# Performance work log

Measured on AMD Instinct MI355X. Metric: run time of the kernel, lower is better.

The kernel has to match this reference:

```python
import jax, jax.numpy as jnp
import numpy as np


def setup_inputs() -> dict:
    key = jax.random.key(0)
    B = 64          # number of utterances (segments)
    N = 16384       # total frames = sum(segment_num)
    D = 1024        # embedding_size
    A = 2048        # attention_dim
    H = 8           # attention_head_num
    k1, k2, k3, k4 = jax.random.split(key, 4)
    # ragged segment lengths, all >= 1, summing exactly to N
    rng = np.random.default_rng(0)
    lens = rng.integers(64, 512, size=B).astype(np.float64)
    lens = np.maximum(1, (lens * N / lens.sum()).astype(np.int64))
    lens[-1] += N - lens.sum()
    assert lens.sum() == N and (lens > 0).all()
    segment_num = jnp.asarray(lens, dtype=jnp.int32)
    x = jax.random.normal(k1, (N, D), jnp.float32)
    # torch Linear weights, stored pre-transposed as [in, out]
    w1 = jax.random.normal(k2, (D, A), jnp.float32) / np.sqrt(D)
    w2 = jax.random.normal(k3, (A, H), jnp.float32) / np.sqrt(A)
    # post_fc: Linear(D*H -> D, bias=False), stored as [D*H, D]
    w_post = jax.random.normal(k4, (D * H, D), jnp.float32) / np.sqrt(D * H)
    return {"x": x, "segment_num": segment_num, "w1": w1, "w2": w2, "w_post": w_post}


def reference(x, segment_num, w1, w2, w_post):
    N, D = x.shape
    B = segment_num.shape[0]
    H = w2.shape[1]
    # segment id for every frame (ragged -> flat segment ids)
    seg_ids = jnp.repeat(jnp.arange(B), segment_num, total_repeat_length=N)  # [N]

    # MultiAtt.w1: Linear -> ReLU -> Linear, per frame
    h = jnp.maximum(x @ w1, 0.0) @ w2  # [N, H]

    # per-segment softmax over the time axis (dim 0 within each segment)
    m = jax.ops.segment_max(h, seg_ids, num_segments=B)          # [B, H]
    p = jnp.exp(h - m[seg_ids])                                  # [N, H]
    s = jax.ops.segment_sum(p, seg_ids, num_segments=B)          # [B, H]
    attn = p / s[seg_ids]                                        # [N, H]

    # per-segment x^T @ attn -> [B, D, H] (matches torch.mm(x.T, attn))
    out_bdh = jax.ops.segment_sum(x[:, :, None] * attn[:, None, :], seg_ids, num_segments=B)
    # flatten row-major over (D, H) like out.view(-1), then post_fc (no bias)
    out = out_bdh.reshape(B, D * H) @ w_post                     # [B, D]

    # attn_i = attn^T @ attn per segment -> [B, H, H]
    attn_gram = jax.ops.segment_sum(attn[:, :, None] * attn[:, None, :], seg_ids, num_segments=B)

    # segment_type == 'average': per-segment mean of frames -> [B, D]
    out_segment = jax.ops.segment_sum(x, seg_ids, num_segments=B) / segment_num[:, None].astype(x.dtype)

    return out, out_segment, attn_gram
```

## Files before the change

kernel.cpp:

```cpp
#include <hip/hip_runtime.h>
#include <hip/hip_bf16.h>

#define NB 64
#define NN 16384
#define ND 1024
#define NA 2048
#define NH 8
#define NSLOT 16
#define KSPL 64
#define NPL 16

typedef __attribute__((ext_vector_type(4))) float f32x4;
typedef __attribute__((ext_vector_type(8))) short short8;
typedef __attribute__((ext_vector_type(8))) unsigned short ushort8;

__device__ __forceinline__ unsigned short f2bf(float f) {
    unsigned int u = __float_as_uint(f);
    u = (u + 0x7fff + ((u >> 16) & 1)) >> 16;
    return (unsigned short)u;
}

__device__ __forceinline__ float bf2f(unsigned short s) {
    return __uint_as_float((unsigned int)s << 16);
}

__device__ __forceinline__ void load_lds16(const void* g, void* l) {
    __builtin_amdgcn_global_load_lds((const __attribute__((address_space(1))) void*)g,
                                     (__attribute__((address_space(3))) void*)l, 16, 0, 0);
}

__global__ __launch_bounds__(256) void k_pre(const float* __restrict__ x,
                                             const float* __restrict__ w1,
                                             const int* __restrict__ segnum,
                                             unsigned short* __restrict__ xb,
                                             unsigned short* __restrict__ w1t,
                                             int* __restrict__ segoff) {
    __shared__ unsigned short t[32][33];
    const int bx = blockIdx.x;
    if (bx < 8192) {
        size_t i = ((size_t)bx * 256 + threadIdx.x) * 8;
        float4 a = *(const float4*)(x + i);
        float4 b = *(const float4*)(x + i + 4);
        ushort8 o;
        o[0] = f2bf(a.x); o[1] = f2bf(a.y); o[2] = f2bf(a.z); o[3] = f2bf(a.w);
        o[4] = f2bf(b.x); o[5] = f2bf(b.y); o[6] = f2bf(b.z); o[7] = f2bf(b.w);
        *(ushort8*)(xb + i) = o;
    } else if (bx < 10240) {
        const int idx = bx - 8192;
        const int a0 = (idx & 63) * 32, d0 = (idx >> 6) * 32;
        const int tx = threadIdx.x & 31, ty4 = (threadIdx.x >> 5) * 4;
#pragma unroll
        for (int i = 0; i < 4; i++)
            t[tx][ty4 + i] = f2bf(w1[(size_t)(d0 + ty4 + i) * NA + a0 + tx]);
        __syncthreads();
#pragma unroll
        for (int i = 0; i < 4; i++)
            w1t[(size_t)(a0 + ty4 + i) * ND + d0 + tx] = t[ty4 + i][tx];
    } else {
        if (threadIdx.x == 0) {
            int a = 0;
            segoff[0] = 0;
            for (int b = 0; b < NB; b++) { a += segnum[b]; segoff[b + 1] = a; }
        }
    }
}

__global__ __launch_bounds__(256) void k_c1h(const unsigned short* __restrict__ xb,
                                             const unsigned short* __restrict__ w1t,
                                             const float* __restrict__ w2,
                                             float* __restrict__ h_part) {
    __shared__ unsigned short SM[21760];
    unsigned short* As  = SM;
    unsigned short* Bs  = SM + 8192;
    unsigned short* c1s = SM;
    unsigned short* w2hi = SM + 17408;
    unsigned short* w2lo = SM + 19584;

    const int tid = threadIdx.x;
    const int wave = tid >> 6, lane = tid & 63;
    const int wm = wave & 1, wn = wave >> 1;
    const int m0 = blockIdx.x * 128, n0 = blockIdx.y * 128;
    const int quad = lane >> 4, lc = lane & 15;

    for (int i = tid; i < 2176; i += 256) { w2hi[i] = 0; w2lo[i] = 0; }
    for (int i = tid; i < 1024; i += 256) {
        int k = i >> 3, q = i & 7;
        float w = w2[(size_t)(n0 + k) * NH + q];
        unsigned short hi = f2bf(w);
        w2hi[q * 136 + k] = hi;
        w2lo[q * 136 + k] = f2bf(w - bf2f(hi));
    }

    f32x4 acc[4][4];
#pragma unroll
    for (int i = 0; i < 4; i++)
#pragma unroll
        for (int j = 0; j < 4; j++) acc[i][j] = (f32x4){0.f, 0.f, 0.f, 0.f};

    const int srow = lane >> 3;
    const int sg = lane & 7;

    for (int k0 = 0; k0 < ND; k0 += 64) {
        __syncthreads();
#pragma unroll
        for (int i = 0; i < 4; i++) {
            int r = wave * 32 + i * 8 + srow;
            int gc = (sg ^ (r & 7)) * 8;
            load_lds16(xb + (size_t)(m0 + r) * ND + k0 + gc, As + r * 64 + sg * 8);
            load_lds16(w1t + (size_t)(n0 + r) * ND + k0 + gc, Bs + r * 64 + sg * 8);
        }
        __syncthreads();
#pragma unroll
        for (int ksub = 0; ksub < 2; ksub++) {
            short8 af[4], bf[4];
            const int lg = ksub * 4 + quad;
#pragma unroll
            for (int t = 0; t < 4; t++) {
                int m = wm * 64 + t * 16 + lc;
                af[t] = *(const short8*)&As[m * 64 + (lg ^ (m & 7)) * 8];
                int n = wn * 64 + t * 16 + lc;
                bf[t] = *(const short8*)&Bs[n * 64 + (lg ^ (n & 7)) * 8];
            }
#pragma unroll
            for (int mi = 0; mi < 4; mi++)
#pragma unroll
                for (int ni = 0; ni < 4; ni++)
                    acc[mi][ni] = __builtin_amdgcn_mfma_f32_16x16x32_bf16(
                        af[mi], bf[ni], acc[mi][ni], 0, 0, 0);
        }
    }

    __syncthreads();
#pragma unroll
    for (int mi = 0; mi < 4; mi++)
#pragma unroll
        for (int ni = 0; ni < 4; ni++) {
            const int col = wn * 64 + ni * 16 + lc;
#pragma unroll
            for (int r = 0; r < 4; r++) {
                const int row = wm * 64 + mi * 16 + quad * 4 + r;
                c1s[row * 136 + col] = f2bf(fmaxf(acc[mi][ni][r], 0.f));
            }
        }
    __syncthreads();

    f32x4 hacc[2];
    hacc[0] = (f32x4){0.f, 0.f, 0.f, 0.f};
    hacc[1] = (f32x4){0.f, 0.f, 0.f, 0.f};
#pragma unroll
    for (int ks = 0; ks < 4; ks++) {
        short8 bh = *(const short8*)&w2hi[lc * 136 + ks * 32 + quad * 8];
        short8 bl = *(const short8*)&w2lo[lc * 136 + ks * 32 + quad * 8];
#pragma unroll
        for (int mt = 0; mt < 2; mt++) {
            short8 af = *(const short8*)&c1s[(wave * 32 + mt * 16 + lc) * 136 + ks * 32 + quad * 8];
            hacc[mt] = __builtin_amdgcn_mfma_f32_16x16x32_bf16(af, bh, hacc[mt], 0, 0, 0);
            hacc[mt] = __builtin_amdgcn_mfma_f32_16x16x32_bf16(af, bl, hacc[mt], 0, 0, 0);
        }
    }

    if (lc < NH) {
        float* hp = h_part + (size_t)blockIdx.y * (NN * NH);
#pragma unroll
        for (int mt = 0; mt < 2; mt++)
#pragma unroll
            for (int r = 0; r < 4; r++)
                hp[(size_t)(m0 + wave * 32 + mt * 16 + quad * 4 + r) * NH + lc] = hacc[mt][r];
    }
}

__global__ __launch_bounds__(256) void k_attn(const float* __restrict__ h_part,
                                              float* __restrict__ attn,
                                              const int* __restrict__ segoff,
                                              float* __restrict__ gram) {
    const int b = blockIdx.x;
    const int s0 = segoff[b], s1 = segoff[b + 1];
    const int len = s1 - s0;
    const int tid = threadIdx.x;
    const int wv = tid >> 6;
    __shared__ float hl[1024 * NH];
    __shared__ float red[4][NH];
    __shared__ float mb[NH];
    __shared__ float sinv[NH];
    __shared__ float gred[4][64];

    float mx[NH];
#pragma unroll
    for (int q = 0; q < NH; q++) mx[q] = -1e30f;

    const bool cached = (len <= 1024);

    for (int n = s0 + tid; n < s1; n += 256) {
        float v[NH];
#pragma unroll
        for (int q = 0; q < NH; q++) v[q] = 0.f;
#pragma unroll
        for (int p = 0; p < NPL; p++) {
            const float4* hp = (const float4*)(h_part + (size_t)p * (NN * NH) + (size_t)n * NH);
            float4 u0 = hp[0], u1 = hp[1];
            v[0] += u0.x; v[1] += u0.y; v[2] += u0.z; v[3] += u0.w;
            v[4] += u1.x; v[5] += u1.y; v[6] += u1.z; v[7] += u1.w;
        }
        if (cached) {
#pragma unroll
            for (int q = 0; q < NH; q++) hl[(n - s0) * NH + q] = v[q];
        }
#pragma unroll
        for (int q = 0; q < NH; q++) mx[q] = fmaxf(mx[q], v[q]);
    }
#pragma unroll
    for (int q = 0; q < NH; q++)
        for (int o = 1; o < 64; o <<= 1) mx[q] = fmaxf(mx[q], __shfl_xor(mx[q], o));
    if ((tid & 63) == 0)
        for (int q = 0; q < NH; q++) red[wv][q] = mx[q];
    __syncthreads();
    if (tid < NH)
        mb[tid] = fmaxf(fmaxf(red[0][tid], red[1][tid]), fmaxf(red[2][tid], red[3][tid]));
    __syncthreads();

    float sm[NH];
#pragma unroll
    for (int q = 0; q < NH; q++) sm[q] = 0.f;
    for (int n = s0 + tid; n < s1; n += 256) {
        float v[NH];
        if (cached) {
#pragma unroll
            for (int q = 0; q < NH; q++) v[q] = hl[(n - s0) * NH + q];
        } else {
#pragma unroll
            for (int q = 0; q < NH; q++) v[q] = 0.f;
#pragma unroll
            for (int p = 0; p < NPL; p++) {
                const float4* hp = (const float4*)(h_part + (size_t)p * (NN * NH) + (size_t)n * NH);
                float4 u0 = hp[0], u1 = hp[1];
                v[0] += u0.x; v[1] += u0.y; v[2] += u0.z; v[3] += u0.w;
                v[4] += u1.x; v[5] += u1.y; v[6] += u1.z; v[7] += u1.w;
            }
        }
#pragma unroll
        for (int q = 0; q < NH; q++) sm[q] += expf(v[q] - mb[q]);
    }
#pragma unroll
    for (int q = 0; q < NH; q++)
        for (int o = 1; o < 64; o <<= 1) sm[q] += __shfl_xor(sm[q], o);
    if ((tid & 63) == 0)
        for (int q = 0; q < NH; q++) red[wv][q] = sm[q];
    __syncthreads();
    if (tid < NH)
        sinv[tid] = 1.0f / (red[0][tid] + red[1][tid] + red[2][tid] + red[3][tid]);
    __syncthreads();

    float g[NH][NH];
#pragma unroll
    for (int i = 0; i < NH; i++)
#pragma unroll
        for (int j = 0; j < NH; j++) g[i][j] = 0.f;

    for (int n = s0 + tid; n < s1; n += 256) {
        float v[NH];
        if (cached) {
#pragma unroll
            for (int q = 0; q < NH; q++) v[q] = hl[(n - s0) * NH + q];
        } else {
#pragma unroll
            for (int q = 0; q < NH; q++) v[q] = 0.f;
#pragma unroll
            for (int p = 0; p < NPL; p++) {
                const float4* hp = (const float4*)(h_part + (size_t)p * (NN * NH) + (size_t)n * NH);
                float4 u0 = hp[0], u1 = hp[1];
                v[0] += u0.x; v[1] += u0.y; v[2] += u0.z; v[3] += u0.w;
                v[4] += u1.x; v[5] += u1.y; v[6] += u1.z; v[7] += u1.w;
            }
        }
        float a[NH];
        float* ar = &attn[(size_t)n * NH];
#pragma unroll
        for (int q = 0; q < NH; q++) { a[q] = expf(v[q] - mb[q]) * sinv[q]; ar[q] = a[q]; }
#pragma unroll
        for (int i = 0; i < NH; i++)
#pragma unroll
            for (int j = 0; j < NH; j++) g[i][j] += a[i] * a[j];
    }
#pragma unroll
    for (int i = 0; i < NH; i++)
#pragma unroll
        for (int j = 0; j < NH; j++)
            for (int o = 1; o < 64; o <<= 1) g[i][j] += __shfl_xor(g[i][j], o);

    if ((tid & 63) == 0) {
#pragma unroll
        for (int i = 0; i < NH; i++)
#pragma unroll
            for (int j = 0; j < NH; j++) gred[wv][i * NH + j] = g[i][j];
    }
    __syncthreads();
    if (tid < 64)
        gram[(size_t)b * 64 + tid] = gred[0][tid] + gred[1][tid] + gred[2][tid] + gred[3][tid];
}

__global__ __launch_bounds__(128) void k_bdh(const unsigned short* __restrict__ xb,
                                             const float* __restrict__ attn,
                                             const int* __restrict__ segoff,
                                             float* __restrict__ bdh_part,
                                             float* __restrict__ xsum_part) {
    const int slot = blockIdx.x;
    const int b = blockIdx.y;
    const int s0 = segoff[b], s1 = segoff[b + 1];
    const int dl = threadIdx.x;

    float acc[8][NH];
    float xs[8];
#pragma unroll
    for (int dd = 0; dd < 8; dd++) {
        xs[dd] = 0.f;
#pragma unroll
        for (int q = 0; q < NH; q++) acc[dd][q] = 0.f;
    }

    for (int n = s0 + slot; n < s1; n += NSLOT) {
        ushort8 xv = *(const ushort8*)(xb + (size_t)n * ND + dl * 8);
        const float4* ap = (const float4*)&attn[(size_t)n * NH];
        float4 a0 = ap[0], a1 = ap[1];
        float aq[NH] = {a0.x, a0.y, a0.z, a0.w, a1.x, a1.y, a1.z, a1.w};
#pragma unroll
        for (int dd = 0; dd < 8; dd++) {
            float xf = bf2f(xv[dd]);
            xs[dd] += xf;
#pragma unroll
            for (int q = 0; q < NH; q++) acc[dd][q] += xf * aq[q];
        }
    }

    float* bp = bdh_part + ((size_t)slot * NB + b) * (ND * NH) + (size_t)dl * 64;
#pragma unroll
    for (int dd = 0; dd < 8; dd++) {
        *(float4*)(bp + dd * 8)     = make_float4(acc[dd][0], acc[dd][1], acc[dd][2], acc[dd][3]);
        *(float4*)(bp + dd * 8 + 4) = make_float4(acc[dd][4], acc[dd][5], acc[dd][6], acc[dd][7]);
    }
    float* xp = xsum_part + ((size_t)slot * NB + b) * ND + (size_t)dl * 8;
    *(float4*)(xp)     = make_float4(xs[0], xs[1], xs[2], xs[3]);
    *(float4*)(xp + 4) = make_float4(xs[4], xs[5], xs[6], xs[7]);
}

__global__ __launch_bounds__(256) void k_bdh_red(const float* __restrict__ bdh_part,
                                                 const float* __restrict__ xsum_part,
                                                 const int* __restrict__ segoff,
                                                 float* __restrict__ bdh,
                                                 float* __restrict__ out_segment) {
    const int gid = blockIdx.x * 256 + threadIdx.x;
    const int b = gid >> 10, d = gid & 1023;
    float4 sa = make_float4(0.f, 0.f, 0.f, 0.f);
    float4 sb = make_float4(0.f, 0.f, 0.f, 0.f);
    float xsum = 0.f;
#pragma unroll
    for (int s = 0; s < NSLOT; s++) {
        const float* p = bdh_part + ((size_t)s * NB + b) * (ND * NH) + (size_t)d * NH;
        float4 u = ((const float4*)p)[0], v = ((const float4*)p)[1];
        sa.x += u.x; sa.y += u.y; sa.z += u.z; sa.w += u.w;
        sb.x += v.x; sb.y += v.y; sb.z += v.z; sb.w += v.w;
        xsum += xsum_part[((size_t)s * NB + b) * ND + d];
    }
    float* bp = bdh + (size_t)b * (ND * NH) + (size_t)d * NH;
    ((float4*)bp)[0] = sa;
    ((float4*)bp)[1] = sb;
    const int len = segoff[b + 1] - segoff[b];
    out_segment[(size_t)b * ND + d] = xsum / (float)len;
}

__global__ __launch_bounds__(256) void k_post(const float* __restrict__ bdh,
                                              const float* __restrict__ wp,
                                              float* __restrict__ out_part) {
    __shared__ float as[32][68];
    __shared__ float bs[32][128];
    const int tid = threadIdx.x;
    const int n0 = blockIdx.x * 128;
    const int k0 = blockIdx.y * (8192 / KSPL);
    const int tr = tid >> 4, tc = tid & 15;

    float acc[4][8];
#pragma unroll
    for (int i = 0; i < 4; i++)
#pragma unroll
        for (int j = 0; j < 8; j++) acc[i][j] = 0.f;

    for (int kc = 0; kc < 8192 / KSPL; kc += 32) {
        __syncthreads();
        {
            int r = tid >> 2;
            int c = (tid & 3) * 8;
            const float4* gp = (const float4*)(bdh + (size_t)r * (ND * NH) + k0 + kc + c);
            float4 v0 = gp[0], v1 = gp[1];
            as[c + 0][r] = v0.x; as[c + 1][r] = v0.y; as[c + 2][r] = v0.z; as[c + 3][r] = v0.w;
            as[c + 4][r] = v1.x; as[c + 5][r] = v1.y; as[c + 6][r] = v1.z; as[c + 7][r] = v1.w;
        }
        {
            int r = tid >> 3;
            int c = (tid & 7) * 16;
            const float4* gp = (const float4*)(wp + (size_t)(k0 + kc + r) * ND + n0 + c);
            float4* sp = (float4*)&bs[r][c];
            sp[0] = gp[0]; sp[1] = gp[1]; sp[2] = gp[2]; sp[3] = gp[3];
        }
        __syncthreads();
#pragma unroll
        for (int k = 0; k < 32; k++) {
            float4 a  = *(const float4*)&as[k][tr * 4];
            float4 b0 = *(const float4*)&bs[k][tc * 8];
            float4 b1 = *(const float4*)&bs[k][tc * 8 + 4];
            float av[4] = {a.x, a.y, a.z, a.w};
            float bv[8] = {b0.x, b0.y, b0.z, b0.w, b1.x, b1.y, b1.z, b1.w};
#pragma unroll
            for (int i = 0; i < 4; i++)
#pragma unroll
                for (int j = 0; j < 8; j++) acc[i][j] += av[i] * bv[j];
        }
    }

    float* op = out_part + (size_t)blockIdx.y * (NB * ND);
#pragma unroll
    for (int i = 0; i < 4; i++)
#pragma unroll
        for (int j = 0; j < 8; j++)
            op[(size_t)(tr * 4 + i) * ND + n0 + tc * 8 + j] = acc[i][j];
}

__global__ __launch_bounds__(256) void k_post_red(const float* __restrict__ out_part,
                                                  float* __restrict__ out) {
    const int i = (blockIdx.x * 256 + threadIdx.x) * 4;
    float4 s = *(const float4*)(out_part + i);
#pragma unroll
    for (int p = 1; p < KSPL; p++) {
        float4 v = *(const float4*)(out_part + (size_t)p * (NB * ND) + i);
        s.x += v.x; s.y += v.y; s.z += v.z; s.w += v.w;
    }
    *(float4*)(out + i) = s;
}

extern "C" void kernel_launch(void* const* d_in, const int* in_sizes, int n_in,
                              void* d_out, int out_size, void* d_ws, size_t ws_size,
                              hipStream_t stream) {
    (void)in_sizes; (void)n_in; (void)out_size; (void)ws_size;
    const float* x      = (const float*)d_in[0];
    const int*   segnum = (const int*)d_in[1];
    const float* w1     = (const float*)d_in[2];
    const float* w2     = (const float*)d_in[3];
    const float* wpost  = (const float*)d_in[4];

    float* out         = (float*)d_out;
    float* out_segment = out + NB * ND;
    float* gram        = out + 2 * NB * ND;

    char* ws = (char*)d_ws;
    const size_t MB = 1024 * 1024;
    int*   segoff   = (int*)ws;
    float* attn     = (float*)(ws + 1 * MB);
    float* bdh      = (float*)(ws + 2 * MB);
    float* h_part   = (float*)(ws + 4 * MB);
    unsigned short* xb  = (unsigned short*)(ws + 12 * MB);
    unsigned short* w1t = (unsigned short*)(ws + 44 * MB);
    float* bdh_part  = (float*)(ws + 48 * MB);
    float* xsum_part = (float*)(ws + 80 * MB);
    float* out_part  = (float*)(ws + 84 * MB);

    k_pre<<<10241, 256, 0, stream>>>(x, w1, segnum, xb, w1t, segoff);
    k_c1h<<<dim3(NN / 128, NA / 128), 256, 0, stream>>>(xb, w1t, w2, h_part);
    k_attn<<<NB, 256, 0, stream>>>(h_part, attn, segoff, gram);
    k_bdh<<<dim3(NSLOT, NB), 128, 0, stream>>>(xb, attn, segoff, bdh_part, xsum_part);
    k_bdh_red<<<256, 256, 0, stream>>>(bdh_part, xsum_part, segoff, bdh, out_segment);
    k_post<<<dim3(ND / 128, KSPL), 256, 0, stream>>>(bdh, wpost, out_part);
    k_post_red<<<(NB * ND) / (256 * 4), 256, 0, stream>>>(out_part, out);
}
```

Baseline: 283.8 us.

## Fuse attention softmax, gram and segment x^T·attn into one per-segment kernel

Replaces the attn, bdh and bdh_red kernels with a single k_seg kernel launched over (8 D-chunks × 64 segments). Each block recomputes the segment softmax from h_part into LDS, and chunk 0 also computes the gram matrix. It then accumulates x^T·attn and the frame sum for its 128-column slice, reducing across 8 frame groups in LDS. This removes the global attn buffer, the 16-slot partial buffers and two launches, at the cost of each of the 8 D-chunk blocks redundantly recomputing the softmax. Only 512 blocks run, and the gram work is serial inside one block per segment.

```diff
diff --git a/kernel.cpp b/kernel.cpp
--- a/kernel.cpp
+++ b/kernel.cpp
@@ -6,9 +6,9 @@
 #define ND 1024
 #define NA 2048
 #define NH 8
-#define NSLOT 16
 #define KSPL 64
 #define NPL 16
+#define MAXL 1024
 
 typedef __attribute__((ext_vector_type(4))) float f32x4;
 typedef __attribute__((ext_vector_type(8))) short short8;
@@ -27,6 +27,18 @@
 __device__ __forceinline__ void load_lds16(const void* g, void* l) {
     __builtin_amdgcn_global_load_lds((const __attribute__((address_space(1))) void*)g,
                                      (__attribute__((address_space(3))) void*)l, 16, 0, 0);
+}
+
+__device__ __forceinline__ void hsum_row(const float* __restrict__ h_part, int n, float* v) {
+#pragma unroll
+    for (int q = 0; q < NH; q++) v[q] = 0.f;
+#pragma unroll
+    for (int p = 0; p < NPL; p++) {
+        const float4* hp = (const float4*)(h_part + (size_t)p * (NN * NH) + (size_t)n * NH);
+        float4 u0 = hp[0], u1 = hp[1];
+        v[0] += u0.x; v[1] += u0.y; v[2] += u0.z; v[3] += u0.w;
+        v[4] += u1.x; v[5] += u1.y; v[6] += u1.z; v[7] += u1.w;
+    }
 }
 
 __global__ __launch_bounds__(256) void k_pre(const float* __restrict__ x,
@@ -169,42 +181,45 @@
     }
 }
 
-__global__ __launch_bounds__(256) void k_attn(const float* __restrict__ h_part,
-                                              float* __restrict__ attn,
-                                              const int* __restrict__ segoff,
-                                              float* __restrict__ gram) {
-    const int b = blockIdx.x;
+__global__ __launch_bounds__(256) void k_seg(const float* __restrict__ h_part,
+                                             const unsigned short* __restrict__ xb,
+                                             const int* __restrict__ segoff,
+                                             float* __restrict__ bdh,
+                                             float* __restrict__ out_segment,
+                                             float* __restrict__ gram) {
+    const int dc = blockIdx.x;
+    const int b  = blockIdx.y;
     const int s0 = segoff[b], s1 = segoff[b + 1];
     const int len = s1 - s0;
+    const int cap = len < MAXL ? len : MAXL;
     const int tid = threadIdx.x;
     const int wv = tid >> 6;
-    __shared__ float hl[1024 * NH];
-    __shared__ float red[4][NH];
-    __shared__ float mb[NH];
-    __shared__ float sinv[NH];
-    __shared__ float gred[4][64];
+
+    __shared__ float hl[MAXL * NH];
+    __shared__ float redf[8 * 32 * 33];
+    __shared__ float xsred[8][132];
+    __shared__ float red[4][NH], mb[NH], sinv[NH], gred[4][64];
+
+    for (int i = tid; i < cap * 2; i += 256) {
+        float4 s = make_float4(0.f, 0.f, 0.f, 0.f);
+#pragma unroll
+        for (int p = 0; p < NPL; p++) {
+            float4 u = *((const float4*)(h_part + (size_t)p * (NN * NH)) + (size_t)s0 * 2 + i);
+            s.x += u.x; s.y += u.y; s.z += u.z; s.w += u.w;
+        }
+        ((float4*)hl)[i] = s;
+    }
+    __syncthreads();
 
     float mx[NH];
 #pragma unroll
     for (int q = 0; q < NH; q++) mx[q] = -1e30f;
-
-    const bool cached = (len <= 1024);
-
-    for (int n = s0 + tid; n < s1; n += 256) {
+    for (int r = tid; r < len; r += 256) {
         float v[NH];
-#pragma unroll
-        for (int q = 0; q < NH; q++) v[q] = 0.f;
-#pragma unroll
-        for (int p = 0; p < NPL; p++) {
-            const float4* hp = (const float4*)(h_part + (size_t)p * (NN * NH) + (size_t)n * NH);
-            float4 u0 = hp[0], u1 = hp[1];
-            v[0] += u0.x; v[1] += u0.y; v[2] += u0.z; v[3] += u0.w;
-            v[4] += u1.x; v[5] += u1.y; v[6] += u1.z; v[7] += u1.w;
-        }
-        if (cached) {
-#pragma unroll
-            for (int q = 0; q < NH; q++) hl[(n - s0) * NH + q] = v[q];
-        }
+        if (r < MAXL) {
+#pragma unroll
+            for (int q = 0; q < NH; q++) v[q] = hl[r * NH + q];
+        } else hsum_row(h_part, s0 + r, v);
 #pragma unroll
         for (int q = 0; q < NH; q++) mx[q] = fmaxf(mx[q], v[q]);
     }
@@ -221,22 +236,12 @@
     float sm[NH];
 #pragma unroll
     for (int q = 0; q < NH; q++) sm[q] = 0.f;
-    for (int n = s0 + tid; n < s1; n += 256) {
+    for (int r = tid; r < len; r += 256) {
         float v[NH];
-        if (cached) {
-#pragma unroll
-            for (int q = 0; q < NH; q++) v[q] = hl[(n - s0) * NH + q];
-        } else {
-#pragma unroll
-            for (int q = 0; q < NH; q++) v[q] = 0.f;
-#pragma unroll
-            for (int p = 0; p < NPL; p++) {
-                const float4* hp = (const float4*)(h_part + (size_t)p * (NN * NH) + (size_t)n * NH);
-                float4 u0 = hp[0], u1 = hp[1];
-                v[0] += u0.x; v[1] += u0.y; v[2] += u0.z; v[3] += u0.w;
-                v[4] += u1.x; v[5] += u1.y; v[6] += u1.z; v[7] += u1.w;
-            }
-        }
+        if (r < MAXL) {
+#pragma unroll
+            for (int q = 0; q < NH; q++) v[q] = hl[r * NH + q];
+        } else hsum_row(h_part, s0 + r, v);
 #pragma unroll
         for (int q = 0; q < NH; q++) sm[q] += expf(v[q] - mb[q]);
     }
@@ -250,121 +255,111 @@
         sinv[tid] = 1.0f / (red[0][tid] + red[1][tid] + red[2][tid] + red[3][tid]);
     __syncthreads();
 
-    float g[NH][NH];
-#pragma unroll
-    for (int i = 0; i < NH; i++)
-#pragma unroll
-        for (int j = 0; j < NH; j++) g[i][j] = 0.f;
-
-    for (int n = s0 + tid; n < s1; n += 256) {
-        float v[NH];
-        if (cached) {
-#pragma unroll
-            for (int q = 0; q < NH; q++) v[q] = hl[(n - s0) * NH + q];
+    for (int r = tid; r < cap; r += 256) {
+#pragma unroll
+        for (int q = 0; q < NH; q++)
+            hl[r * NH + q] = expf(hl[r * NH + q] - mb[q]) * sinv[q];
+    }
+    __syncthreads();
+
+    if (dc == 0) {
+        float g[NH][NH];
+#pragma unroll
+        for (int i = 0; i < NH; i++)
+#pragma unroll
+            for (int j = 0; j < NH; j++) g[i][j] = 0.f;
+        for (int r = tid; r < len; r += 256) {
+            float a[NH];
+            if (r < MAXL) {
+#pragma unroll
+                for (int q = 0; q < NH; q++) a[q] = hl[r * NH + q];
+            } else {
+                hsum_row(h_part, s0 + r, a);
+#pragma unroll
+                for (int q = 0; q < NH; q++) a[q] = expf(a[q] - mb[q]) * sinv[q];
+            }
+#pragma unroll
+            for (int i = 0; i < NH; i++)
+#pragma unroll
+                for (int j = 0; j < NH; j++) g[i][j] += a[i] * a[j];
+        }
+#pragma unroll
+        for (int i = 0; i < NH; i++)
+#pragma unroll
+            for (int j = 0; j < NH; j++)
+                for (int o = 1; o < 64; o <<= 1) g[i][j] += __shfl_xor(g[i][j], o);
+        if ((tid & 63) == 0) {
+#pragma unroll
+            for (int i = 0; i < NH; i++)
+#pragma unroll
+                for (int j = 0; j < NH; j++) gred[wv][i * NH + j] = g[i][j];
+        }
+        __syncthreads();
+        if (tid < 64)
+            gram[(size_t)b * 64 + tid] = gred[0][tid] + gred[1][tid] + gred[2][tid] + gred[3][tid];
+    }
+
+    const int fo = tid >> 5, dg = tid & 31;
+    const int d = dc * 128 + dg * 4;
+    float acc[4][NH];
+    float xs4[4] = {0.f, 0.f, 0.f, 0.f};
+#pragma unroll
+    for (int dd = 0; dd < 4; dd++)
+#pragma unroll
+        for (int q = 0; q < NH; q++) acc[dd][q] = 0.f;
+
+    for (int n = fo; n < len; n += 8) {
+        ushort4 xv = *(const ushort4*)(xb + (size_t)(s0 + n) * ND + d);
+        float a[NH];
+        if (n < MAXL) {
+            const float4* ap = (const float4*)&hl[n * NH];
+            float4 a0 = ap[0], a1 = ap[1];
+            a[0] = a0.x; a[1] = a0.y; a[2] = a0.z; a[3] = a0.w;
+            a[4] = a1.x; a[5] = a1.y; a[6] = a1.z; a[7] = a1.w;
         } else {
-#pragma unroll
-            for (int q = 0; q < NH; q++) v[q] = 0.f;
-#pragma unroll
-            for (int p = 0; p < NPL; p++) {
-                const float4* hp = (const float4*)(h_part + (size_t)p * (NN * NH) + (size_t)n * NH);
-                float4 u0 = hp[0], u1 = hp[1];
-                v[0] += u0.x; v[1] += u0.y; v[2] += u0.z; v[3] += u0.w;
-                v[4] += u1.x; v[5] += u1.y; v[6] += u1.z; v[7] += u1.w;
-            }
-        }
-        float a[NH];
-        float* ar = &attn[(size_t)n * NH];
-#pragma unroll
-        for (int q = 0; q < NH; q++) { a[q] = expf(v[q] - mb[q]) * sinv[q]; ar[q] = a[q]; }
-#pragma unroll
-        for (int i = 0; i < NH; i++)
-#pragma unroll
-            for (int j = 0; j < NH; j++) g[i][j] += a[i] * a[j];
-    }
-#pragma unroll
-    for (int i = 0; i < NH; i++)
-#pragma unroll
-        for (int j = 0; j < NH; j++)
-            for (int o = 1; o < 64; o <<= 1) g[i][j] += __shfl_xor(g[i][j], o);
-
-    if ((tid & 63) == 0) {
-#pragma unroll
-        for (int i = 0; i < NH; i++)
-#pragma unroll
-            for (int j = 0; j < NH; j++) gred[wv][i * NH + j] = g[i][j];
-    }
-    __syncthreads();
-    if (tid < 64)
-        gram[(size_t)b * 64 + tid] = gred[0][tid] + gred[1][tid] + gred[2][tid] + gred[3][tid];
-}
-
-__global__ __launch_bounds__(128) void k_bdh(const unsigned short* __restrict__ xb,
-                                             const float* __restrict__ attn,
-                                             const int* __restrict__ segoff,
-                                             float* __restrict__ bdh_part,
-                                             float* __restrict__ xsum_part) {
-    const int slot = blockIdx.x;
-    const int b = blockIdx.y;
-    const int s0 = segoff[b], s1 = segoff[b + 1];
-    const int dl = threadIdx.x;
-
-    float acc[8][NH];
-    float xs[8];
-#pragma unroll
-    for (int dd = 0; dd < 8; dd++) {
-        xs[dd] = 0.f;
-#pragma unroll
-        for (int q = 0; q < NH; q++) acc[dd][q] = 0.f;
-    }
-
-    for (int n = s0 + slot; n < s1; n += NSLOT) {
-        ushort8 xv = *(const ushort8*)(xb + (size_t)n * ND + dl * 8);
-        const float4* ap = (const float4*)&attn[(size_t)n * NH];
-        float4 a0 = ap[0], a1 = ap[1];
-        float aq[NH] = {a0.x, a0.y, a0.z, a0.w, a1.x, a1.y, a1.z, a1.w};
-#pragma unroll
-        for (int dd = 0; dd < 8; dd++) {
-            float xf = bf2f(xv[dd]);
-            xs[dd] += xf;
-#pragma unroll
-            for (int q = 0; q < NH; q++) acc[dd][q] += xf * aq[q];
-        }
-    }
-
-    float* bp = bdh_part + ((size_t)slot * NB + b) * (ND * NH) + (size_t)dl * 64;
-#pragma unroll
-    for (int dd = 0; dd < 8; dd++) {
-        *(float4*)(bp + dd * 8)     = make_float4(acc[dd][0], acc[dd][1], acc[dd][2], acc[dd][3]);
-        *(float4*)(bp + dd * 8 + 4) = make_float4(acc[dd][4], acc[dd][5], acc[dd][6], acc[dd][7]);
-    }
-    float* xp = xsum_part + ((size_t)slot * NB + b) * ND + (size_t)dl * 8;
-    *(float4*)(xp)     = make_float4(xs[0], xs[1], xs[2], xs[3]);
-    *(float4*)(xp + 4) = make_float4(xs[4], xs[5], xs[6], xs[7]);
-}
-
-__global__ __launch_bounds__(256) void k_bdh_red(const float* __restrict__ bdh_part,
-                                                 const float* __restrict__ xsum_part,
-                                                 const int* __restrict__ segoff,
-                                                 float* __restrict__ bdh,
-                                                 float* __restrict__ out_segment) {
-    const int gid = blockIdx.x * 256 + threadIdx.x;
-    const int b = gid >> 10, d = gid & 1023;
-    float4 sa = make_float4(0.f, 0.f, 0.f, 0.f);
-    float4 sb = make_float4(0.f, 0.f, 0.f, 0.f);
-    float xsum = 0.f;
-#pragma unroll
-    for (int s = 0; s < NSLOT; s++) {
-        const float* p = bdh_part + ((size_t)s * NB + b) * (ND * NH) + (size_t)d * NH;
-        float4 u = ((const float4*)p)[0], v = ((const float4*)p)[1];
-        sa.x += u.x; sa.y += u.y; sa.z += u.z; sa.w += u.w;
-        sb.x += v.x; sb.y += v.y; sb.z += v.z; sb.w += v.w;
-        xsum += xsum_part[((size_t)s * NB + b) * ND + d];
-    }
-    float* bp = bdh + (size_t)b * (ND * NH) + (size_t)d * NH;
-    ((float4*)bp)[0] = sa;
-    ((float4*)bp)[1] = sb;
-    const int len = segoff[b + 1] - segoff[b];
-    out_segment[(size_t)b * ND + d] = xsum / (float)len;
+            hsum_row(h_part, s0 + n, a);
+#pragma unroll
+            for (int q = 0; q < NH; q++) a[q] = expf(a[q] - mb[q]) * sinv[q];
+        }
+        float xf[4] = {bf2f(xv.x), bf2f(xv.y), bf2f(xv.z), bf2f(xv.w)};
+#pragma unroll
+        for (int dd = 0; dd < 4; dd++) {
+            xs4[dd] += xf[dd];
+#pragma unroll
+            for (int q = 0; q < NH; q++) acc[dd][q] += xf[dd] * a[q];
+        }
+    }
+
+    {
+        float* rp = redf + (fo * 32 + dg) * 33;
+#pragma unroll
+        for (int dd = 0; dd < 4; dd++)
+#pragma unroll
+            for (int q = 0; q < NH; q++) rp[dd * 8 + q] = acc[dd][q];
+#pragma unroll
+        for (int dd = 0; dd < 4; dd++) xsred[fo][dg * 4 + dd] = xs4[dd];
+    }
+    __syncthreads();
+    {
+        float ov[4];
+#pragma unroll
+        for (int j = 0; j < 4; j++) {
+            int o = tid * 4 + j;
+            int g = o >> 5, e = o & 31;
+            float s = 0.f;
+#pragma unroll
+            for (int f = 0; f < 8; f++) s += redf[(f * 32 + g) * 33 + e];
+            ov[j] = s;
+        }
+        *(float4*)(bdh + (size_t)b * (ND * NH) + (size_t)dc * 1024 + tid * 4) =
+            make_float4(ov[0], ov[1], ov[2], ov[3]);
+        if (tid < 128) {
+            float s = 0.f;
+#pragma unroll
+            for (int f = 0; f < 8; f++) s += xsred[f][tid];
+            out_segment[(size_t)b * ND + dc * 128 + tid] = s / (float)len;
+        }
+    }
 }
 
 __global__ __launch_bounds__(256) void k_post(const float* __restrict__ bdh,
@@ -452,20 +447,15 @@
     char* ws = (char*)d_ws;
     const size_t MB = 1024 * 1024;
     int*   segoff   = (int*)ws;
-    float* attn     = (float*)(ws + 1 * MB);
     float* bdh      = (float*)(ws + 2 * MB);
     float* h_part   = (float*)(ws + 4 * MB);
     unsigned short* xb  = (unsigned short*)(ws + 12 * MB);
     unsigned short* w1t = (unsigned short*)(ws + 44 * MB);
-    float* bdh_part  = (float*)(ws + 48 * MB);
-    float* xsum_part = (float*)(ws + 80 * MB);
-    float* out_part  = (float*)(ws + 84 * MB);
+    float* out_part  = (float*)(ws + 48 * MB);
 
     k_pre<<<10241, 256, 0, stream>>>(x, w1, segnum, xb, w1t, segoff);
     k_c1h<<<dim3(NN / 128, NA / 128), 256, 0, stream>>>(xb, w1t, w2, h_part);
-    k_attn<<<NB, 256, 0, stream>>>(h_part, attn, segoff, gram);
-    k_bdh<<<dim3(NSLOT, NB), 128, 0, stream>>>(xb, attn, segoff, bdh_part, xsum_part);
-    k_bdh_red<<<256, 256, 0, stream>>>(bdh_part, xsum_part, segoff, bdh, out_segment);
+    k_seg<<<dim3(8, NB), 256, 0, stream>>>(h_part, xb, segoff, bdh, out_segment, gram);
     k_post<<<dim3(ND / 128, KSPL), 256, 0, stream>>>(bdh, wpost, out_part);
     k_post_red<<<(NB * ND) / (256 * 4), 256, 0, stream>>>(out_part, out);
 }
```

New measurement: 284.7 us. About the same (+0.3%).
